# Optimization experiments

Hardware: AMD Instinct MI355X
Metric: run time of the kernel (lower is better)

## Reference

```python
import jax, jax.numpy as jnp
import numpy as np
from jax import lax

B, CIN, COUT, H, W = 4, 256, 256, 64, 64
K = 3  # kernel size
PAD = 1
STRIDE = 1


def setup_inputs() -> dict:
    key = jax.random.key(0)
    k1, k2, k3, k4 = jax.random.split(key, 4)
    x = jax.random.normal(k1, (B, CIN, H, W), dtype=jnp.float32)
    # small offset weights so learned offsets are modest (original init is zeros)
    offset_w = jax.random.normal(k2, (3 * K * K, CIN, K, K), dtype=jnp.float32) * 0.01
    offset_b = jax.random.normal(k3, (3 * K * K,), dtype=jnp.float32) * 0.01
    dcn_w = jax.random.normal(k4, (COUT, CIN, K, K), dtype=jnp.float32) * (1.0 / np.sqrt(CIN * K * K))
    return {"x": x, "offset_w": offset_w, "offset_b": offset_b, "dcn_w": dcn_w}


def _dcnv2(x, offset_w, offset_b, dcn_w):
    b, c, h, w = x.shape
    kk = K * K
    # offset conv (standard 3x3, stride 1, pad 1)
    o = lax.conv_general_dilated(
        x, offset_w, (STRIDE, STRIDE), ((PAD, PAD), (PAD, PAD)),
        dimension_numbers=("NCHW", "OIHW", "NCHW"))
    o = o + offset_b[None, :, None, None]
    ho, wo = o.shape[2], o.shape[3]
    off = o[:, : 2 * kk].reshape(b, kk, 2, ho, wo)  # pairs are (dy, dx)
    dy, dx = off[:, :, 0], off[:, :, 1]             # [b,kk,ho,wo]
    mask = jax.nn.sigmoid(o[:, 2 * kk:])            # [b,kk,ho,wo]

    ki, kj = jnp.meshgrid(jnp.arange(K), jnp.arange(K), indexing="ij")
    ki = ki.reshape(kk).astype(jnp.float32)
    kj = kj.reshape(kk).astype(jnp.float32)
    base_y = (jnp.arange(ho, dtype=jnp.float32) * STRIDE - PAD)[None, None, :, None] + ki[None, :, None, None]
    base_x = (jnp.arange(wo, dtype=jnp.float32) * STRIDE - PAD)[None, None, None, :] + kj[None, :, None, None]
    py = base_y + dy  # [b,kk,ho,wo] sampling y
    px = base_x + dx  # sampling x

    y0 = jnp.floor(py)
    x0 = jnp.floor(px)
    wy = py - y0  # bilinear fractional weights
    wx = px - x0
    y0i = y0.astype(jnp.int32)
    x0i = x0.astype(jnp.int32)

    xT = x.transpose(0, 2, 3, 1)  # [b,h,w,c] for channel-last gathers
    bidx = jnp.arange(b)[:, None, None, None]

    def gather(yi, xi):
        # zero padding outside the image
        valid = (yi >= 0) & (yi < h) & (xi >= 0) & (xi < w)
        yc = jnp.clip(yi, 0, h - 1)
        xc = jnp.clip(xi, 0, w - 1)
        v = xT[bidx, yc, xc]  # [b,kk,ho,wo,c]
        return v * valid[..., None].astype(x.dtype)

    g00 = gather(y0i, x0i)
    g01 = gather(y0i, x0i + 1)
    g10 = gather(y0i + 1, x0i)
    g11 = gather(y0i + 1, x0i + 1)

    wy_ = wy[..., None]
    wx_ = wx[..., None]
    sampled = (g00 * (1 - wy_) * (1 - wx_) + g01 * (1 - wy_) * wx_
               + g10 * wy_ * (1 - wx_) + g11 * wy_ * wx_)
    sampled = sampled * mask[..., None]  # modulation

    wk = dcn_w.reshape(dcn_w.shape[0], c, kk)  # [o,c,kk]
    return jnp.einsum("bkhwc,ock->bohw", sampled, wk)


def reference(x, offset_w, offset_b, dcn_w):
    return _dcnv2(x, offset_w, offset_b, dcn_w)
```

## Files before the change

kernel.cpp:

```cpp
#include <hip/hip_runtime.h>
#include <hip/hip_bf16.h>
#include <stdint.h>
#include <math.h>

#define KDIM 2304

typedef __attribute__((ext_vector_type(8))) short bf16x8;
typedef __attribute__((ext_vector_type(4))) float f32x4;

__device__ inline unsigned short f2bf(float f) {
  union { float f; unsigned int u; } v; v.f = f;
  unsigned int u = v.u;
  unsigned int r = (u + 0x7FFFu + ((u >> 16) & 1u)) >> 16;
  return (unsigned short)r;
}
__device__ inline float bf2f(unsigned short h) {
  union { unsigned int u; float f; } v; v.u = ((unsigned int)h) << 16;
  return v.f;
}

__device__ inline void gl2lds16(const void* g, void* l) {
  __builtin_amdgcn_global_load_lds((const __attribute__((address_space(1))) void*)g,
                                   (__attribute__((address_space(3))) void*)l,
                                   16, 0, 0);
}

__global__ __launch_bounds__(256) void k_transpose(const float* __restrict__ x,
                                                   unsigned short* __restrict__ xTb) {
  __shared__ float tile[32][33];
  int t = threadIdx.x;
  int tx = t & 31, ty = t >> 5;
  int p0 = blockIdx.x * 32;
  int c0 = blockIdx.y * 32;
  int b  = blockIdx.z;
  const float* xb = x + ((size_t)b << 20);
#pragma unroll
  for (int i = 0; i < 4; ++i) {
    int c = c0 + ty + i * 8;
    tile[ty + i * 8][tx] = xb[((size_t)c << 12) + p0 + tx];
  }
  __syncthreads();
  unsigned short* ob = xTb + ((size_t)b << 20);
#pragma unroll
  for (int i = 0; i < 4; ++i) {
    int p = p0 + ty + i * 8;
    ob[(((size_t)p) << 8) + c0 + tx] = f2bf(tile[tx][ty + i * 8]);
  }
}

__global__ __launch_bounds__(256) void k_wprep(const float* __restrict__ dcn_w,
                                               const float* __restrict__ offset_w,
                                               unsigned short* __restrict__ Wpk,
                                               unsigned short* __restrict__ Wob,
                                               unsigned short* __restrict__ zp) {
  int gid = blockIdx.x * 256 + threadIdx.x;
  const int N1 = 72 * 8192;
  const int N2 = 32 * KDIM;
  if (gid < N1) {
    int j = gid & 7;
    int lane = (gid >> 3) & 63;
    int mb = (gid >> 9) & 15;
    int kc = gid >> 13;
    int row = mb * 16 + (lane & 15);
    int gk = kc * 32 + ((lane >> 4) << 3) + j;
    int c = gk & 255, kidx = gk >> 8;
    Wpk[gid] = f2bf(dcn_w[((size_t)(row * 256 + c)) * 9 + kidx]);
  } else if (gid < N1 + N2) {
    int g = gid - N1;
    int ch = g / KDIM, k = g % KDIM;
    int kidx = k >> 8, c = k & 255;
    Wob[g] = (ch < 27) ? f2bf(offset_w[((size_t)(ch * 256 + c)) * 9 + kidx])
                       : (unsigned short)0;
  } else if (gid < N1 + N2 + 128) {
    zp[gid - N1 - N2] = 0;
  }
}

__global__ __launch_bounds__(256) void k_offs_gemm(const unsigned short* __restrict__ xTb,
                                                   const unsigned short* __restrict__ Wob,
                                                   const unsigned short* __restrict__ zp,
                                                   float* __restrict__ O2p) {
  __shared__ unsigned short As[64 * 32];
  __shared__ unsigned short Bs[32 * 32];
  int t = threadIdx.x;
  int wv = t >> 6, lane = t & 63;
  int n0 = blockIdx.x * 64;
  int z = blockIdx.y;
  int r0 = t >> 2, coff = (t & 3) * 8;

  int rowA = n0 + r0;
  int b_ = rowA >> 12, hw = rowA & 4095, h = hw >> 6, w = hw & 63;

  f32x4 acc[2] = {};
  char* AsB = (char*)As;
  char* BsB = (char*)Bs;

  for (int kt = z * 36; kt < z * 36 + 36; ++kt) {
    int k0 = kt * 32;
    int kidx = k0 >> 8, c0 = k0 & 255;
    int di = kidx / 3 - 1, dj = kidx % 3 - 1;
    {
      int y = h + di, xx = w + dj;
      const unsigned short* g = (y >= 0 && y < 64 && xx >= 0 && xx < 64)
          ? xTb + (((((size_t)b_) << 12) + (y << 6) + xx) << 8) + c0 + coff
          : zp;
      gl2lds16(g, AsB + wv * 1024);
    }
    if (t < 128) {
      const unsigned short* g = Wob + (size_t)(t >> 2) * KDIM + k0 + coff;
      gl2lds16(g, BsB + wv * 1024);
    }
    __syncthreads();
    bf16x8 aF, bF[2];
    aF = *(const bf16x8*)(As + (wv * 16 + (lane & 15)) * 32 + (lane >> 4) * 8);
#pragma unroll
    for (int j = 0; j < 2; ++j)
      bF[j] = *(const bf16x8*)(Bs + (j * 16 + (lane & 15)) * 32 + (lane >> 4) * 8);
#pragma unroll
    for (int j = 0; j < 2; ++j)
      acc[j] = __builtin_amdgcn_mfma_f32_16x16x32_bf16(aF, bF[j], acc[j], 0, 0, 0);
    __syncthreads();
  }

  int quad = lane >> 4, cl = lane & 15;
  float* O2z = O2p + (size_t)z * 16384 * 32;
#pragma unroll
  for (int j = 0; j < 2; ++j) {
    int col = j * 16 + cl;
#pragma unroll
    for (int r = 0; r < 4; ++r) {
      int row = n0 + wv * 16 + quad * 4 + r;
      O2z[(size_t)row * 32 + col] = acc[j][r];
    }
  }
}

__global__ __launch_bounds__(256) void k_sweights(const float* __restrict__ O2p,
                                                  const float* __restrict__ offb,
                                                  float* __restrict__ SW) {
  int gid = blockIdx.x * 256 + threadIdx.x;
  if (gid >= 9 * 16384) return;
  int k = gid >> 14;
  int bhw = gid & 16383;
  int h = (bhw >> 6) & 63, w = bhw & 63;

  const float* o0 = O2p + (size_t)bhw * 32;
  const float* o1 = o0 + (size_t)16384 * 32;
  float dy = o0[2 * k]     + o1[2 * k]     + offb[2 * k];
  float dx = o0[2 * k + 1] + o1[2 * k + 1] + offb[2 * k + 1];
  float mv = o0[18 + k]    + o1[18 + k]    + offb[18 + k];
  float mask = 1.0f / (1.0f + expf(-mv));

  float py = (float)(h - 1 + k / 3) + dy;
  float px = (float)(w - 1 + k % 3) + dx;
  float y0f = floorf(py), x0f = floorf(px);
  float wy = py - y0f, wx = px - x0f;
  int y0 = (int)y0f, x0 = (int)x0f;
  int y1 = y0 + 1, x1 = x0 + 1;

  float vy0 = (y0 >= 0 && y0 < 64) ? 1.f : 0.f;
  float vy1 = (y1 >= 0 && y1 < 64) ? 1.f : 0.f;
  float vx0 = (x0 >= 0 && x0 < 64) ? 1.f : 0.f;
  float vx1 = (x1 >= 0 && x1 < 64) ? 1.f : 0.f;
  int y0c = min(max(y0, 0), 63), y1c = min(max(y1, 0), 63);
  int x0c = min(max(x0, 0), 63), x1c = min(max(x1, 0), 63);

  float4 wv4;
  wv4.x = (1.f - wy) * (1.f - wx) * vy0 * vx0 * mask;
  wv4.y = (1.f - wy) * wx * vy0 * vx1 * mask;
  wv4.z = wy * (1.f - wx) * vy1 * vx0 * mask;
  wv4.w = wy * wx * vy1 * vx1 * mask;
  uint4 ov;
  ov.x = (unsigned)(((y0c << 6) + x0c) << 8);
  ov.y = (unsigned)(((y0c << 6) + x1c) << 8);
  ov.z = (unsigned)(((y1c << 6) + x0c) << 8);
  ov.w = (unsigned)(((y1c << 6) + x1c) << 8);

  float* p = SW + (size_t)gid * 8;
  *(float4*)p = wv4;
  *(uint4*)(p + 4) = ov;
}

__global__ __launch_bounds__(512) void k_fused(const unsigned short* __restrict__ Wpk,
                                               const unsigned short* __restrict__ xTb,
                                               const float* __restrict__ SW,
                                               float* __restrict__ out) {
  __shared__ __align__(16) unsigned short Bs[2][64 * 40];
  int t = threadIdx.x;
  int wv = t >> 6, lane = t & 63;
  int wm = wv & 3, wn = wv >> 2;
  int n0 = blockIdx.x * 64;
  int b  = n0 >> 12;
  const unsigned short* xb = xTb + ((size_t)b << 20);

  int r = t >> 3, g = t & 7;
  int ch0 = g * 4;
  int bsw = r * 40 + ch0;

  const unsigned short* wpBase = Wpk + ((size_t)(wm * 4 * 64 + lane)) * 8;

  f32x4 acc[4][2] = {};

  float4 wv4; uint4 ov;
  {
    const float* sw = SW + ((size_t)(n0 + r)) * 8;
    wv4 = *(const float4*)sw;
    ov  = *(const uint4*)(sw + 4);
  }
  ushort4 q00, q01, q10, q11;
  bf16x8 aF[4], aFn[4];

  {
    unsigned c = (unsigned)ch0;
    q00 = *(const ushort4*)(xb + ov.x + c);
    q01 = *(const ushort4*)(xb + ov.y + c);
    q10 = *(const ushort4*)(xb + ov.z + c);
    q11 = *(const ushort4*)(xb + ov.w + c);
#pragma unroll
    for (int i = 0; i < 4; ++i)
      aF[i] = *(const bf16x8*)(wpBase + (size_t)i * 512);
  }

#pragma unroll 2
  for (int kt = 0; kt < 72; ++kt) {
    float s[4];
    s[0] = wv4.x * bf2f(q00.x) + wv4.y * bf2f(q01.x) + wv4.z * bf2f(q10.x) + wv4.w * bf2f(q11.x);
    s[1] = wv4.x * bf2f(q00.y) + wv4.y * bf2f(q01.y) + wv4.z * bf2f(q10.y) + wv4.w * bf2f(q11.y);
    s[2] = wv4.x * bf2f(q00.z) + wv4.y * bf2f(q01.z) + wv4.z * bf2f(q10.z) + wv4.w * bf2f(q11.z);
    s[3] = wv4.x * bf2f(q00.w) + wv4.y * bf2f(q01.w) + wv4.z * bf2f(q10.w) + wv4.w * bf2f(q11.w);
    union { __hip_bfloat162 h2[2]; ushort4 v; } pk;
    pk.h2[0] = __float22bfloat162_rn(make_float2(s[0], s[1]));
    pk.h2[1] = __float22bfloat162_rn(make_float2(s[2], s[3]));
    *(ushort4*)(&Bs[kt & 1][bsw]) = pk.v;

    if (kt < 71) {
      int kn = kt + 1;
      if ((kn & 7) == 0) {
        const float* sw = SW + ((size_t)(((kn >> 3) << 14) + n0 + r)) * 8;
        wv4 = *(const float4*)sw;
        ov  = *(const uint4*)(sw + 4);
      }
      unsigned c = (unsigned)(((kn & 7) << 5) + ch0);
      q00 = *(const ushort4*)(xb + ov.x + c);
      q01 = *(const ushort4*)(xb + ov.y + c);
      q10 = *(const ushort4*)(xb + ov.z + c);
      q11 = *(const ushort4*)(xb + ov.w + c);
#pragma unroll
      for (int i = 0; i < 4; ++i)
        aFn[i] = *(const bf16x8*)(wpBase + ((size_t)kn * 16 + i) * 512);
    }

    __syncthreads();
    bf16x8 bF[2];
#pragma unroll
    for (int j = 0; j < 2; ++j)
      bF[j] = *(const bf16x8*)(&Bs[kt & 1][(wn * 32 + j * 16 + (lane & 15)) * 40 + (lane >> 4) * 8]);
#pragma unroll
    for (int i = 0; i < 4; ++i)
#pragma unroll
      for (int j = 0; j < 2; ++j)
        acc[i][j] = __builtin_amdgcn_mfma_f32_16x16x32_bf16(aF[i], bF[j], acc[i][j], 0, 0, 0);
    if (kt < 71) {
#pragma unroll
      for (int i = 0; i < 4; ++i) aF[i] = aFn[i];
    }
  }

  int quad = lane >> 4, cl = lane & 15;
  float* ob = out + (((size_t)b) << 20);
#pragma unroll
  for (int i = 0; i < 4; ++i) {
    int mbase = wm * 64 + i * 16 + quad * 4;
#pragma unroll
    for (int j = 0; j < 2; ++j) {
      int hw = (n0 & 4095) + wn * 32 + j * 16 + cl;
      float* op = ob + hw;
#pragma unroll
      for (int rr = 0; rr < 4; ++rr)
        op[((size_t)(mbase + rr)) << 12] = acc[i][j][rr];
    }
  }
}

extern "C" void kernel_launch(void* const* d_in, const int* in_sizes, int n_in,
                              void* d_out, int out_size, void* d_ws, size_t ws_size,
                              hipStream_t stream) {
  const float* x        = (const float*)d_in[0];
  const float* offset_w = (const float*)d_in[1];
  const float* offset_b = (const float*)d_in[2];
  const float* dcn_w    = (const float*)d_in[3];
  float* out = (float*)d_out;

  char* ws = (char*)d_ws;
  size_t off = 0;
  auto carve = [&](size_t bytes) -> void* {
    void* p = ws + off;
    off += (bytes + 255) & ~(size_t)255;
    return p;
  };
  unsigned short* xTb = (unsigned short*)carve(4ull * 64 * 64 * 256 * 2);
  unsigned short* Wpk = (unsigned short*)carve(72ull * 8192 * 2);
  unsigned short* Wob = (unsigned short*)carve(32ull * KDIM * 2);
  unsigned short* zp  = (unsigned short*)carve(256);
  float*          O2p = (float*)carve(2ull * 16384 * 32 * 4);
  float*          SW  = (float*)carve(9ull * 16384 * 8 * 4);
  (void)ws_size; (void)in_sizes; (void)n_in; (void)out_size;

  k_transpose<<<dim3(128, 8, 4), 256, 0, stream>>>(x, xTb);
  k_wprep<<<dim3((72 * 8192 + 32 * KDIM + 128 + 255) / 256), 256, 0, stream>>>(
      dcn_w, offset_w, Wpk, Wob, zp);
  k_offs_gemm<<<dim3(256, 2), 256, 0, stream>>>(xTb, Wob, zp, O2p);
  k_sweights<<<dim3((9 * 16384 + 255) / 256), 256, 0, stream>>>(O2p, offset_b, SW);
  k_fused<<<dim3(256), 512, 0, stream>>>(Wpk, xTb, SW, out);
}
```

Baseline: 153.6 us.

## Double-buffer offset GEMM LDS loads and prefetch sampling weights earlier

The offset-conv GEMM now double-buffers its A/B LDS tiles, issuing the next tile's global-to-LDS loads before computing the current one and using explicit vmcnt waits with raw barriers instead of __syncthreads. The main deformable GEMM prefetches the next kidx group's sampling weights and offsets seven iterations ahead, so the dependent gather no longer waits on them. It also replaces __syncthreads there with an lgkmcnt wait plus s_barrier, which no longer drains outstanding global loads. The hand-written waitcnt counts are fragile: if the compiler reorders or adds memory ops, the buffers could be read before their data has arrived.

```diff
diff --git a/kernel.cpp b/kernel.cpp
--- a/kernel.cpp
+++ b/kernel.cpp
@@ -80,8 +80,8 @@
                                                    const unsigned short* __restrict__ Wob,
                                                    const unsigned short* __restrict__ zp,
                                                    float* __restrict__ O2p) {
-  __shared__ unsigned short As[64 * 32];
-  __shared__ unsigned short Bs[32 * 32];
+  __shared__ unsigned short As[2][64 * 32];
+  __shared__ unsigned short Bs[2][32 * 32];
   int t = threadIdx.x;
   int wv = t >> 6, lane = t & 63;
   int n0 = blockIdx.x * 64;
@@ -92,34 +92,46 @@
   int b_ = rowA >> 12, hw = rowA & 4095, h = hw >> 6, w = hw & 63;
 
   f32x4 acc[2] = {};
-  char* AsB = (char*)As;
-  char* BsB = (char*)Bs;
-
-  for (int kt = z * 36; kt < z * 36 + 36; ++kt) {
+
+  auto stage = [&](int kt, int buf) {
     int k0 = kt * 32;
     int kidx = k0 >> 8, c0 = k0 & 255;
     int di = kidx / 3 - 1, dj = kidx % 3 - 1;
-    {
-      int y = h + di, xx = w + dj;
-      const unsigned short* g = (y >= 0 && y < 64 && xx >= 0 && xx < 64)
-          ? xTb + (((((size_t)b_) << 12) + (y << 6) + xx) << 8) + c0 + coff
-          : zp;
-      gl2lds16(g, AsB + wv * 1024);
-    }
+    int y = h + di, xx = w + dj;
+    const unsigned short* g = (y >= 0 && y < 64 && xx >= 0 && xx < 64)
+        ? xTb + (((((size_t)b_) << 12) + (y << 6) + xx) << 8) + c0 + coff
+        : zp;
+    gl2lds16(g, (char*)As[buf] + wv * 1024);
     if (t < 128) {
-      const unsigned short* g = Wob + (size_t)(t >> 2) * KDIM + k0 + coff;
-      gl2lds16(g, BsB + wv * 1024);
-    }
-    __syncthreads();
+      const unsigned short* gB = Wob + (size_t)(t >> 2) * KDIM + k0 + coff;
+      gl2lds16(gB, (char*)Bs[buf] + wv * 1024);
+    }
+  };
+
+  int kbeg = z * 36, kend = kbeg + 36;
+  stage(kbeg, 0);
+
+  for (int kt = kbeg; kt < kend; ++kt) {
+    int buf = (kt - kbeg) & 1;
+    if (kt + 1 < kend) {
+      stage(kt + 1, buf ^ 1);
+      if (wv < 2) asm volatile("s_waitcnt vmcnt(2)" ::: "memory");
+      else        asm volatile("s_waitcnt vmcnt(1)" ::: "memory");
+    } else {
+      asm volatile("s_waitcnt vmcnt(0)" ::: "memory");
+    }
+    asm volatile("s_barrier" ::: "memory");
+
     bf16x8 aF, bF[2];
-    aF = *(const bf16x8*)(As + (wv * 16 + (lane & 15)) * 32 + (lane >> 4) * 8);
+    aF = *(const bf16x8*)(As[buf] + (wv * 16 + (lane & 15)) * 32 + (lane >> 4) * 8);
 #pragma unroll
     for (int j = 0; j < 2; ++j)
-      bF[j] = *(const bf16x8*)(Bs + (j * 16 + (lane & 15)) * 32 + (lane >> 4) * 8);
+      bF[j] = *(const bf16x8*)(Bs[buf] + (j * 16 + (lane & 15)) * 32 + (lane >> 4) * 8);
 #pragma unroll
     for (int j = 0; j < 2; ++j)
       acc[j] = __builtin_amdgcn_mfma_f32_16x16x32_bf16(aF, bF[j], acc[j], 0, 0, 0);
-    __syncthreads();
+
+    asm volatile("s_barrier" ::: "memory");
   }
 
   int quad = lane >> 4, cl = lane & 15;
@@ -207,6 +219,7 @@
     wv4 = *(const float4*)sw;
     ov  = *(const uint4*)(sw + 4);
   }
+  float4 wv4n = wv4; uint4 ovn = ov;
   ushort4 q00, q01, q10, q11;
   bf16x8 aF[4], aFn[4];
 
@@ -233,13 +246,15 @@
     pk.h2[1] = __float22bfloat162_rn(make_float2(s[2], s[3]));
     *(ushort4*)(&Bs[kt & 1][bsw]) = pk.v;
 
+    if ((kt & 7) == 0 && kt < 64) {
+      const float* swp = SW + ((size_t)((((kt >> 3) + 1) << 14) + n0 + r)) * 8;
+      wv4n = *(const float4*)swp;
+      ovn  = *(const uint4*)(swp + 4);
+    }
+
     if (kt < 71) {
       int kn = kt + 1;
-      if ((kn & 7) == 0) {
-        const float* sw = SW + ((size_t)(((kn >> 3) << 14) + n0 + r)) * 8;
-        wv4 = *(const float4*)sw;
-        ov  = *(const uint4*)(sw + 4);
-      }
+      if ((kn & 7) == 0) { wv4 = wv4n; ov = ovn; }
       unsigned c = (unsigned)(((kn & 7) << 5) + ch0);
       q00 = *(const ushort4*)(xb + ov.x + c);
       q01 = *(const ushort4*)(xb + ov.y + c);
@@ -250,7 +265,8 @@
         aFn[i] = *(const bf16x8*)(wpBase + ((size_t)kn * 16 + i) * 512);
     }
 
-    __syncthreads();
+    asm volatile("s_waitcnt lgkmcnt(0)\n\ts_barrier" ::: "memory");
+
     bf16x8 bF[2];
 #pragma unroll
     for (int j = 0; j < 2; ++j)
```

After: 156.1 us. About the same (+1.6%).
